# Kernel optimization log

Hardware: AMD Instinct MI355X
Metric: run time of the kernel (lower is better)

## Reference

```python
import jax, jax.numpy as jnp
import numpy as np
import math

D = 1024      # size_kernel
H = 16        # num_heads
HD = D // H   # head_dim
PAD = 1       # pad_index
B, S = 8, 1024


def setup_inputs() -> dict:
    key = jax.random.key(0)
    ks = jax.random.split(key, 10)
    scale = 1.0 / math.sqrt(D)
    x = jax.random.normal(ks[0], (B, S, D), dtype=jnp.float32)
    input_ids = jax.random.randint(ks[1], (B, S), 0, 10000, dtype=jnp.int64)
    Wq = jax.random.uniform(ks[2], (D, D), jnp.float32, -scale, scale)
    bq = jax.random.uniform(ks[3], (D,), jnp.float32, -scale, scale)
    Wk = jax.random.uniform(ks[4], (D, D), jnp.float32, -scale, scale)
    bk = jax.random.uniform(ks[5], (D,), jnp.float32, -scale, scale)
    Wv = jax.random.uniform(ks[6], (D, D), jnp.float32, -scale, scale)
    bv = jax.random.uniform(ks[7], (D,), jnp.float32, -scale, scale)
    Wo = jax.random.uniform(ks[8], (D, D), jnp.float32, -scale, scale)
    bo = jax.random.uniform(ks[9], (D,), jnp.float32, -scale, scale)
    return {"x": x, "input_ids": input_ids, "Wq": Wq, "bq": bq,
            "Wk": Wk, "bk": bk, "Wv": Wv, "bv": bv, "Wo": Wo, "bo": bo}


def reference(x, input_ids, Wq, bq, Wk, bk, Wv, bv, Wo, bo):
    b, s, _ = x.shape
    # QKV projections -> [b, h, s, hd]
    def split_heads(t):
        return t.reshape(b, s, H, HD).transpose(0, 2, 1, 3)
    q = split_heads(x @ Wq.T + bq)
    k = split_heads(x @ Wk.T + bk)
    v = split_heads(x @ Wv.T + bv)
    # scores [b, h, s, s]
    scores = jnp.einsum('bhqd,bhkd->bhqk', q, k) / math.sqrt(HD)
    pad_mask = (input_ids != PAD)[:, None, None, :]          # [b,1,1,s] keys
    causal = jnp.tril(jnp.ones((s, s), dtype=bool))[None, None]  # [1,1,s,s]
    mask = pad_mask & causal
    min_val = jnp.finfo(scores.dtype).min
    scores = jnp.where(mask, scores, min_val)
    attn = jax.nn.softmax(scores, axis=-1)
    out = jnp.einsum('bhqk,bhkd->bhqd', attn, v)             # [b,h,s,hd]
    out = out.transpose(0, 2, 1, 3).reshape(b, s, D)
    return out @ Wo.T + bo
```

## Files before the change

kernel.cpp:

```cpp
#include <hip/hip_runtime.h>

typedef __attribute__((ext_vector_type(8))) short bf16x8;
typedef __attribute__((ext_vector_type(8))) unsigned short u16x8;
typedef __attribute__((ext_vector_type(4))) unsigned short u16x4;
typedef __attribute__((ext_vector_type(4))) float f32x4;
typedef unsigned short u16t;

#define MFMA16(a, b, c) __builtin_amdgcn_mfma_f32_16x16x32_bf16((a), (b), (c), 0, 0, 0)
#define GLDS16(gp, lp)                                                        \
  __builtin_amdgcn_global_load_lds(                                           \
      (__attribute__((address_space(1))) void*)(gp),                          \
      (__attribute__((address_space(3))) void*)(lp), 16, 0, 0)

static constexpr float L2E = 1.44269504f;
static constexpr float MASKV = -1.0e30f;

__device__ __forceinline__ u16t f2b(float f) {
  unsigned u = __builtin_bit_cast(unsigned, f);
  u = u + 0x7fffu + ((u >> 16) & 1u);
  return (u16t)(u >> 16);
}

__global__ void cvt5(const float* __restrict__ x, const float* __restrict__ wq,
                     const float* __restrict__ wk, const float* __restrict__ wv,
                     const float* __restrict__ wo, u16t* __restrict__ xb,
                     u16t* __restrict__ wqb, u16t* __restrict__ wkb,
                     u16t* __restrict__ wvb, u16t* __restrict__ wob) {
  const int bid = blockIdx.x;
  const float* src; u16t* dst; int gb;
  if (bid < 4096)      { src = x;  dst = xb;  gb = bid; }
  else if (bid < 4608) { src = wq; dst = wqb; gb = bid - 4096; }
  else if (bid < 5120) { src = wk; dst = wkb; gb = bid - 4608; }
  else if (bid < 5632) { src = wv; dst = wvb; gb = bid - 5120; }
  else                 { src = wo; dst = wob; gb = bid - 5632; }
  const size_t i = (size_t)gb * 256 + threadIdx.x;
  const float4 a = ((const float4*)src)[2 * i];
  const float4 b = ((const float4*)src)[2 * i + 1];
  u16x8 r;
  r[0] = f2b(a.x); r[1] = f2b(a.y); r[2] = f2b(a.z); r[3] = f2b(a.w);
  r[4] = f2b(b.x); r[5] = f2b(b.y); r[6] = f2b(b.z); r[7] = f2b(b.w);
  *(u16x8*)&dst[8 * i] = r;
}

__global__ void gemm_qkv(const u16t* __restrict__ X,
                         const u16t* __restrict__ Wq, const u16t* __restrict__ Wk,
                         const u16t* __restrict__ Wv,
                         const float* __restrict__ bq, const float* __restrict__ bk,
                         const float* __restrict__ bv,
                         u16t* __restrict__ Qo, u16t* __restrict__ Ko,
                         u16t* __restrict__ Vo) {
  __shared__ __align__(16) u16t As[128 * 32];
  __shared__ __align__(16) u16t Bs[128 * 32];
  const int t = threadIdx.x, lane = t & 63, w = t >> 6;
  const int wr = w >> 1, wc = w & 1, m = lane & 15, quad = lane >> 4;
  const int rowBase = blockIdx.y * 128, colBase = blockIdx.x * 128;
  const int z = blockIdx.z;
  const u16t* W = (z == 0) ? Wq : ((z == 1) ? Wk : Wv);
  const float* bias = (z == 0) ? bq : ((z == 1) ? bk : bv);
  u16t* Out = (z == 0) ? Qo : ((z == 1) ? Ko : Vo);

  f32x4 acc[4][4];
#pragma unroll
  for (int i = 0; i < 4; i++)
#pragma unroll
    for (int j = 0; j < 4; j++) acc[i][j] = (f32x4){0.f, 0.f, 0.f, 0.f};

  const int lr = lane >> 2, lc = (lane & 3) * 8;
  for (int kt = 0; kt < 32; ++kt) {
#pragma unroll
    for (int i = 0; i < 2; ++i) {
      const int r0 = i * 64 + w * 16;
      GLDS16(&X[(size_t)(rowBase + r0 + lr) * 1024 + kt * 32 + lc], &As[r0 * 32]);
      GLDS16(&W[(size_t)(colBase + r0 + lr) * 1024 + kt * 32 + lc], &Bs[r0 * 32]);
    }
    __syncthreads();
    bf16x8 af[4], bfr[4];
#pragma unroll
    for (int i = 0; i < 4; i++)
      af[i] = *(const bf16x8*)&As[(wr * 64 + i * 16 + m) * 32 + quad * 8];
#pragma unroll
    for (int j = 0; j < 4; j++)
      bfr[j] = *(const bf16x8*)&Bs[(wc * 64 + j * 16 + m) * 32 + quad * 8];
#pragma unroll
    for (int i = 0; i < 4; i++)
#pragma unroll
      for (int j = 0; j < 4; j++) acc[i][j] = MFMA16(af[i], bfr[j], acc[i][j]);
    __syncthreads();
  }

  const int b_ = rowBase >> 10;
  const int sBase = (rowBase & 1023) + wr * 64;
#pragma unroll
  for (int j = 0; j < 4; j++) {
    const int col = colBase + wc * 64 + j * 16 + m;
    const float bv_ = bias[col];
    const int h = col >> 6, hd = col & 63;
    if (z == 2) {
#pragma unroll
      for (int i = 0; i < 4; i++) {
        const int s0 = sBase + i * 16 + quad * 4;
        u16x4 pk;
#pragma unroll
        for (int r = 0; r < 4; r++) pk[r] = f2b(acc[i][j][r] + bv_);
        *(u16x4*)&Out[(((size_t)b_ * 16 + h) * 64 + hd) * 1024 + s0] = pk;
      }
    } else {
#pragma unroll
      for (int i = 0; i < 4; i++) {
#pragma unroll
        for (int r = 0; r < 4; r++) {
          const int s_ = sBase + i * 16 + quad * 4 + r;
          const size_t oi = (((size_t)b_ * 16 + h) * 1024 + s_) * 64 + hd;
          Out[oi] = f2b(acc[i][j][r] + bv_);
        }
      }
    }
  }
}

__global__ void gemm_o(const u16t* __restrict__ A, const u16t* __restrict__ W,
                       const float* __restrict__ bias, float* __restrict__ Out) {
  __shared__ __align__(16) u16t As[128 * 32];
  __shared__ __align__(16) u16t Bs[128 * 32];
  const int t = threadIdx.x, lane = t & 63, w = t >> 6;
  const int wr = w >> 1, wc = w & 1, m = lane & 15, quad = lane >> 4;
  const int rowBase = blockIdx.y * 128, colBase = blockIdx.x * 128;

  f32x4 acc[4][4];
#pragma unroll
  for (int i = 0; i < 4; i++)
#pragma unroll
    for (int j = 0; j < 4; j++) acc[i][j] = (f32x4){0.f, 0.f, 0.f, 0.f};

  const int lr = lane >> 2, lc = (lane & 3) * 8;
  for (int kt = 0; kt < 32; ++kt) {
#pragma unroll
    for (int i = 0; i < 2; ++i) {
      const int r0 = i * 64 + w * 16;
      GLDS16(&A[(size_t)(rowBase + r0 + lr) * 1024 + kt * 32 + lc], &As[r0 * 32]);
      GLDS16(&W[(size_t)(colBase + r0 + lr) * 1024 + kt * 32 + lc], &Bs[r0 * 32]);
    }
    __syncthreads();
    bf16x8 af[4], bfr[4];
#pragma unroll
    for (int i = 0; i < 4; i++)
      af[i] = *(const bf16x8*)&As[(wr * 64 + i * 16 + m) * 32 + quad * 8];
#pragma unroll
    for (int j = 0; j < 4; j++)
      bfr[j] = *(const bf16x8*)&Bs[(wc * 64 + j * 16 + m) * 32 + quad * 8];
#pragma unroll
    for (int i = 0; i < 4; i++)
#pragma unroll
      for (int j = 0; j < 4; j++) acc[i][j] = MFMA16(af[i], bfr[j], acc[i][j]);
    __syncthreads();
  }

#pragma unroll
  for (int j = 0; j < 4; j++) {
    const int col = colBase + wc * 64 + j * 16 + m;
    const float bv_ = bias[col];
#pragma unroll
    for (int i = 0; i < 4; i++) {
#pragma unroll
      for (int r = 0; r < 4; r++) {
        const int row = rowBase + wr * 64 + i * 16 + quad * 4 + r;
        Out[(size_t)row * 1024 + col] = acc[i][j][r] + bv_;
      }
    }
  }
}

__global__ __launch_bounds__(512) void attn(
    const u16t* __restrict__ Q, const u16t* __restrict__ K,
    const u16t* __restrict__ VT, const int* __restrict__ ids,
    u16t* __restrict__ Oo) {
  constexpr int PSTR = 72;
  __shared__ __align__(16) u16t Kb[2][64 * 64];
  __shared__ __align__(16) u16t Vb[2][64 * 64];
  __shared__ __align__(16) u16t Ps[8][16 * PSTR];
  __shared__ unsigned long long maskL[16];

  const int t = threadIdx.x, lane = t & 63, wl = t >> 6;
  const int m = lane & 15, quad = lane >> 4;
  const int id = blockIdx.x;
  const int g = id & 7, k_ = id >> 3;
  const int bh = g + 8 * (k_ & 15);
  const int p4 = k_ >> 4;
  const int b = bh >> 4, h = bh & 15;
  const size_t hoff = (size_t)bh * 65536;

  const int srow = lane >> 3;
  const int sg = (lane & 7) ^ (srow & 7);

#pragma unroll
  for (int c = 0; c < 2; ++c) {
    const int chunk = wl * 2 + c;
    const int idv = ids[b * 1024 + chunk * 64 + lane];
    const unsigned long long mk = __ballot(idv != 1);
    if (lane == 0) maskL[chunk] = mk;
  }
  __syncthreads();

  u16t* const Pw = &Ps[wl][0];

  for (int pass = 0; pass < 2; ++pass) {
    const int qt8 = pass ? (7 - p4) : p4;
    const int qbase = qt8 * 128 + wl * 16;
    const int qrow = qbase + m;
    const int ktmax = 2 * qt8 + 1;

    GLDS16(&K[hoff + (size_t)(wl * 8 + srow) * 64 + sg * 8], &Kb[0][wl * 512]);
    GLDS16(&VT[hoff + (size_t)(wl * 8 + srow) * 1024 + sg * 8], &Vb[0][wl * 512]);

    const bf16x8 qf0 =
        *(const bf16x8*)&Q[hoff + (size_t)(qbase + m) * 64 + quad * 8];
    const bf16x8 qf1 =
        *(const bf16x8*)&Q[hoff + (size_t)(qbase + m) * 64 + 32 + quad * 8];

    float mi = MASKV, li = 0.f;
    f32x4 o[4];
#pragma unroll
    for (int ot = 0; ot < 4; ot++) o[ot] = (f32x4){0.f, 0.f, 0.f, 0.f};

    __syncthreads();

    for (int kt = 0; kt <= ktmax; ++kt) {
      if (kt < ktmax) {
        u16t* const kb = &Kb[(kt + 1) & 1][wl * 512];
        u16t* const vb = &Vb[(kt + 1) & 1][wl * 512];
        GLDS16(&K[hoff + (size_t)((kt + 1) * 64 + wl * 8 + srow) * 64 + sg * 8], kb);
        GLDS16(&VT[hoff + (size_t)(wl * 8 + srow) * 1024 + (kt + 1) * 64 + sg * 8], vb);
      }

      if (kt * 64 <= qbase + 15) {
        const u16t* const Kc = Kb[kt & 1];
        const u16t* const Vc = Vb[kt & 1];

        const int dq0 = qrow - kt * 64;
        const int dqc = dq0 > 63 ? 63 : dq0;
        const unsigned long long causal =
            (dqc == 63) ? ~0ull : ((1ull << (dqc + 1)) - 1ull);
        const unsigned long long km2 = maskL[kt] & causal;
        const unsigned kqlo = (unsigned)(km2 >> (quad * 4));
        const unsigned kqhi = (unsigned)(km2 >> (quad * 4 + 32));

        f32x4 sc[4];
        float pm = MASKV;
#pragma unroll
        for (int nt = 0; nt < 4; nt++) {
          if ((kt * 64 + nt * 16) <= (qbase + 15)) {
            const int krow = (nt * 16 + m) * 64;
            const bf16x8 k0 =
                *(const bf16x8*)&Kc[krow + ((quad ^ (m & 7)) & 7) * 8];
            const bf16x8 k1 =
                *(const bf16x8*)&Kc[krow + (((quad + 4) ^ (m & 7)) & 7) * 8];
            f32x4 c = (f32x4){0.f, 0.f, 0.f, 0.f};
            c = MFMA16(k0, qf0, c);
            c = MFMA16(k1, qf1, c);
            const unsigned w32 = (nt < 2) ? kqlo : kqhi;
#pragma unroll
            for (int r = 0; r < 4; r++) {
              const int sh = (nt & 1) * 16 + r;
              const float s = ((w32 >> sh) & 1u) ? c[r] * 0.125f : MASKV;
              sc[nt][r] = s;
              pm = fmaxf(pm, s);
            }
          } else {
#pragma unroll
            for (int r = 0; r < 4; r++) sc[nt][r] = MASKV;
          }
        }
        pm = fmaxf(pm, __shfl_xor(pm, 16));
        pm = fmaxf(pm, __shfl_xor(pm, 32));

        if (__any(pm > mi + 8.0f)) {
          const float mn = (pm > mi + 8.0f) ? pm : mi;
          const float alpha = exp2f((mi - mn) * L2E);
          mi = mn;
          li *= alpha;
#pragma unroll
          for (int r = 0; r < 4; r++) {
            const float ar = __shfl(alpha, quad * 4 + r);
#pragma unroll
            for (int ot = 0; ot < 4; ot++) o[ot][r] *= ar;
          }
        }

        float rsum = 0.f;
#pragma unroll
        for (int nt = 0; nt < 4; nt++) {
          float pf[4];
#pragma unroll
          for (int r = 0; r < 4; r++) {
            pf[r] = exp2f((sc[nt][r] - mi) * L2E);
            rsum += pf[r];
          }
          unsigned w0, w1;
          asm("v_cvt_pk_bf16_f32 %0, %1, %2" : "=v"(w0) : "v"(pf[0]), "v"(pf[1]));
          asm("v_cvt_pk_bf16_f32 %0, %1, %2" : "=v"(w1) : "v"(pf[2]), "v"(pf[3]));
          uint2 wv; wv.x = w0; wv.y = w1;
          *(uint2*)&Pw[m * PSTR + nt * 16 + quad * 4] = wv;
        }
        rsum += __shfl_xor(rsum, 16);
        rsum += __shfl_xor(rsum, 32);
        li += rsum;

        const bf16x8 p0 = *(const bf16x8*)&Pw[m * PSTR + quad * 8];
        const bf16x8 p1 = *(const bf16x8*)&Pw[m * PSTR + 32 + quad * 8];
#pragma unroll
        for (int ot = 0; ot < 4; ot++) {
          const int vrow = (ot * 16 + m) * 64;
          const bf16x8 v0 =
              *(const bf16x8*)&Vc[vrow + ((quad ^ (m & 7)) & 7) * 8];
          const bf16x8 v1 =
              *(const bf16x8*)&Vc[vrow + (((quad + 4) ^ (m & 7)) & 7) * 8];
          o[ot] = MFMA16(p0, v0, o[ot]);
          o[ot] = MFMA16(p1, v1, o[ot]);
        }
      }

      __syncthreads();
    }

    const float linv = (li > 1e-30f) ? 1.f / li : 0.f;
#pragma unroll
    for (int r = 0; r < 4; r++) {
      const float inv = __shfl(linv, quad * 4 + r);
      const int qo = qbase + quad * 4 + r;
#pragma unroll
      for (int ot = 0; ot < 4; ot++) {
        const int col = h * 64 + ot * 16 + m;
        Oo[((size_t)(b * 1024 + qo)) * 1024 + col] = f2b(o[ot][r] * inv);
      }
    }
  }
}

extern "C" void kernel_launch(void* const* d_in, const int* in_sizes, int n_in,
                              void* d_out, int out_size, void* d_ws, size_t ws_size,
                              hipStream_t stream) {
  const float* x  = (const float*)d_in[0];
  const int*   ids = (const int*)d_in[1];
  const float* Wq = (const float*)d_in[2];
  const float* bq = (const float*)d_in[3];
  const float* Wk = (const float*)d_in[4];
  const float* bk = (const float*)d_in[5];
  const float* Wv = (const float*)d_in[6];
  const float* bv = (const float*)d_in[7];
  const float* Wo = (const float*)d_in[8];
  const float* bo = (const float*)d_in[9];
  float* out = (float*)d_out;

  u16t* XB  = (u16t*)d_ws;
  u16t* WqB = XB  + 8388608;
  u16t* WkB = WqB + 1048576;
  u16t* WvB = WkB + 1048576;
  u16t* WoB = WvB + 1048576;
  u16t* Qw  = WoB + 1048576;
  u16t* Kw  = Qw  + 8388608;
  u16t* Vw  = Kw  + 8388608;
  u16t* AO  = XB;

  cvt5<<<6144, 256, 0, stream>>>(x, Wq, Wk, Wv, Wo, XB, WqB, WkB, WvB, WoB);
  gemm_qkv<<<dim3(8, 64, 3), 256, 0, stream>>>(XB, WqB, WkB, WvB, bq, bk, bv,
                                               Qw, Kw, Vw);
  attn<<<512, 512, 0, stream>>>(Qw, Kw, Vw, ids, AO);
  gemm_o<<<dim3(8, 64, 1), 256, 0, stream>>>(AO, WoB, bo, out);
}
```

Before: 265.3 us.

## Double-buffer GEMM LDS tiles and remap blocks for XCD-local L2 reuse

Both the QKV and output-projection GEMMs now keep two LDS buffers, issuing the global-to-LDS loads for the next K tile before computing on the current one. This drops one barrier per iteration and overlaps load latency with MFMA work. The grids are flattened to 1D and remapped so that blocks landing on the same XCD share row tiles, aiming to improve L2 reuse of the A operand. The cost is double the LDS per block, which could lower occupancy.

```diff
diff --git a/kernel.cpp b/kernel.cpp
--- a/kernel.cpp
+++ b/kernel.cpp
@@ -49,12 +49,16 @@
                          const float* __restrict__ bv,
                          u16t* __restrict__ Qo, u16t* __restrict__ Ko,
                          u16t* __restrict__ Vo) {
-  __shared__ __align__(16) u16t As[128 * 32];
-  __shared__ __align__(16) u16t Bs[128 * 32];
+  __shared__ __align__(16) u16t As[2][128 * 32];
+  __shared__ __align__(16) u16t Bs[2][128 * 32];
   const int t = threadIdx.x, lane = t & 63, w = t >> 6;
   const int wr = w >> 1, wc = w & 1, m = lane & 15, quad = lane >> 4;
-  const int rowBase = blockIdx.y * 128, colBase = blockIdx.x * 128;
-  const int z = blockIdx.z;
+  const int id = blockIdx.x;
+  const int xcd = id & 7, j = id >> 3;
+  const int by = xcd * 8 + (j & 7);
+  const int rem = j >> 3;
+  const int bx = rem & 7, z = rem >> 3;
+  const int rowBase = by * 128, colBase = bx * 128;
   const u16t* W = (z == 0) ? Wq : ((z == 1) ? Wk : Wv);
   const float* bias = (z == 0) ? bq : ((z == 1) ? bk : bv);
   u16t* Out = (z == 0) ? Qo : ((z == 1) ? Ko : Vo);
@@ -63,36 +67,48 @@
 #pragma unroll
   for (int i = 0; i < 4; i++)
 #pragma unroll
-    for (int j = 0; j < 4; j++) acc[i][j] = (f32x4){0.f, 0.f, 0.f, 0.f};
+    for (int j2 = 0; j2 < 4; j2++) acc[i][j2] = (f32x4){0.f, 0.f, 0.f, 0.f};
 
   const int lr = lane >> 2, lc = (lane & 3) * 8;
+#pragma unroll
+  for (int i = 0; i < 2; ++i) {
+    const int r0 = i * 64 + w * 16;
+    GLDS16(&X[(size_t)(rowBase + r0 + lr) * 1024 + lc], &As[0][r0 * 32]);
+    GLDS16(&W[(size_t)(colBase + r0 + lr) * 1024 + lc], &Bs[0][r0 * 32]);
+  }
+  __syncthreads();
+
   for (int kt = 0; kt < 32; ++kt) {
-#pragma unroll
-    for (int i = 0; i < 2; ++i) {
-      const int r0 = i * 64 + w * 16;
-      GLDS16(&X[(size_t)(rowBase + r0 + lr) * 1024 + kt * 32 + lc], &As[r0 * 32]);
-      GLDS16(&W[(size_t)(colBase + r0 + lr) * 1024 + kt * 32 + lc], &Bs[r0 * 32]);
-    }
-    __syncthreads();
+    const int cur = kt & 1;
+    if (kt < 31) {
+#pragma unroll
+      for (int i = 0; i < 2; ++i) {
+        const int r0 = i * 64 + w * 16;
+        GLDS16(&X[(size_t)(rowBase + r0 + lr) * 1024 + (kt + 1) * 32 + lc],
+               &As[cur ^ 1][r0 * 32]);
+        GLDS16(&W[(size_t)(colBase + r0 + lr) * 1024 + (kt + 1) * 32 + lc],
+               &Bs[cur ^ 1][r0 * 32]);
+      }
+    }
     bf16x8 af[4], bfr[4];
 #pragma unroll
     for (int i = 0; i < 4; i++)
-      af[i] = *(const bf16x8*)&As[(wr * 64 + i * 16 + m) * 32 + quad * 8];
-#pragma unroll
-    for (int j = 0; j < 4; j++)
-      bfr[j] = *(const bf16x8*)&Bs[(wc * 64 + j * 16 + m) * 32 + quad * 8];
+      af[i] = *(const bf16x8*)&As[cur][(wr * 64 + i * 16 + m) * 32 + quad * 8];
+#pragma unroll
+    for (int j2 = 0; j2 < 4; j2++)
+      bfr[j2] = *(const bf16x8*)&Bs[cur][(wc * 64 + j2 * 16 + m) * 32 + quad * 8];
 #pragma unroll
     for (int i = 0; i < 4; i++)
 #pragma unroll
-      for (int j = 0; j < 4; j++) acc[i][j] = MFMA16(af[i], bfr[j], acc[i][j]);
+      for (int j2 = 0; j2 < 4; j2++) acc[i][j2] = MFMA16(af[i], bfr[j2], acc[i][j2]);
     __syncthreads();
   }
 
   const int b_ = rowBase >> 10;
   const int sBase = (rowBase & 1023) + wr * 64;
 #pragma unroll
-  for (int j = 0; j < 4; j++) {
-    const int col = colBase + wc * 64 + j * 16 + m;
+  for (int j2 = 0; j2 < 4; j2++) {
+    const int col = colBase + wc * 64 + j2 * 16 + m;
     const float bv_ = bias[col];
     const int h = col >> 6, hd = col & 63;
     if (z == 2) {
@@ -101,7 +117,7 @@
         const int s0 = sBase + i * 16 + quad * 4;
         u16x4 pk;
 #pragma unroll
-        for (int r = 0; r < 4; r++) pk[r] = f2b(acc[i][j][r] + bv_);
+        for (int r = 0; r < 4; r++) pk[r] = f2b(acc[i][j2][r] + bv_);
         *(u16x4*)&Out[(((size_t)b_ * 16 + h) * 64 + hd) * 1024 + s0] = pk;
       }
     } else {
@@ -111,7 +127,7 @@
         for (int r = 0; r < 4; r++) {
           const int s_ = sBase + i * 16 + quad * 4 + r;
           const size_t oi = (((size_t)b_ * 16 + h) * 1024 + s_) * 64 + hd;
-          Out[oi] = f2b(acc[i][j][r] + bv_);
+          Out[oi] = f2b(acc[i][j2][r] + bv_);
         }
       }
     }
@@ -120,51 +136,67 @@
 
 __global__ void gemm_o(const u16t* __restrict__ A, const u16t* __restrict__ W,
                        const float* __restrict__ bias, float* __restrict__ Out) {
-  __shared__ __align__(16) u16t As[128 * 32];
-  __shared__ __align__(16) u16t Bs[128 * 32];
+  __shared__ __align__(16) u16t As[2][128 * 32];
+  __shared__ __align__(16) u16t Bs[2][128 * 32];
   const int t = threadIdx.x, lane = t & 63, w = t >> 6;
   const int wr = w >> 1, wc = w & 1, m = lane & 15, quad = lane >> 4;
-  const int rowBase = blockIdx.y * 128, colBase = blockIdx.x * 128;
+  const int id = blockIdx.x;
+  const int xcd = id & 7, j = id >> 3;
+  const int by = xcd * 8 + (j & 7);
+  const int bx = j >> 3;
+  const int rowBase = by * 128, colBase = bx * 128;
 
   f32x4 acc[4][4];
 #pragma unroll
   for (int i = 0; i < 4; i++)
 #pragma unroll
-    for (int j = 0; j < 4; j++) acc[i][j] = (f32x4){0.f, 0.f, 0.f, 0.f};
+    for (int j2 = 0; j2 < 4; j2++) acc[i][j2] = (f32x4){0.f, 0.f, 0.f, 0.f};
 
   const int lr = lane >> 2, lc = (lane & 3) * 8;
+#pragma unroll
+  for (int i = 0; i < 2; ++i) {
+    const int r0 = i * 64 + w * 16;
+    GLDS16(&A[(size_t)(rowBase + r0 + lr) * 1024 + lc], &As[0][r0 * 32]);
+    GLDS16(&W[(size_t)(colBase + r0 + lr) * 1024 + lc], &Bs[0][r0 * 32]);
+  }
+  __syncthreads();
+
   for (int kt = 0; kt < 32; ++kt) {
-#pragma unroll
-    for (int i = 0; i < 2; ++i) {
-      const int r0 = i * 64 + w * 16;
-      GLDS16(&A[(size_t)(rowBase + r0 + lr) * 1024 + kt * 32 + lc], &As[r0 * 32]);
-      GLDS16(&W[(size_t)(colBase + r0 + lr) * 1024 + kt * 32 + lc], &Bs[r0 * 32]);
-    }
+    const int cur = kt & 1;
+    if (kt < 31) {
+#pragma unroll
+      for (int i = 0; i < 2; ++i) {
+        const int r0 = i * 64 + w * 16;
+        GLDS16(&A[(size_t)(rowBase + r0 + lr) * 1024 + (kt + 1) * 32 + lc],
+               &As[cur ^ 1][r0 * 32]);
+        GLDS16(&W[(size_t)(colBase + r0 + lr) * 1024 + (kt + 1) * 32 + lc],
+               &Bs[cur ^ 1][r0 * 32]);
+      }
+    }
+    bf16x8 af[4], bfr[4];
+#pragma unroll
+    for (int i = 0; i < 4; i++)
+      af[i] = *(const bf16x8*)&As[cur][(wr * 64 + i * 16 + m) * 32 + quad * 8];
+#pragma unroll
+    for (int j2 = 0; j2 < 4; j2++)
+      bfr[j2] = *(const bf16x8*)&Bs[cur][(wc * 64 + j2 * 16 + m) * 32 + quad * 8];
+#pragma unroll
+    for (int i = 0; i < 4; i++)
+#pragma unroll
+      for (int j2 = 0; j2 < 4; j2++) acc[i][j2] = MFMA16(af[i], bfr[j2], acc[i][j2]);
     __syncthreads();
-    bf16x8 af[4], bfr[4];
-#pragma unroll
-    for (int i = 0; i < 4; i++)
-      af[i] = *(const bf16x8*)&As[(wr * 64 + i * 16 + m) * 32 + quad * 8];
-#pragma unroll
-    for (int j = 0; j < 4; j++)
-      bfr[j] = *(const bf16x8*)&Bs[(wc * 64 + j * 16 + m) * 32 + quad * 8];
-#pragma unroll
-    for (int i = 0; i < 4; i++)
-#pragma unroll
-      for (int j = 0; j < 4; j++) acc[i][j] = MFMA16(af[i], bfr[j], acc[i][j]);
-    __syncthreads();
-  }
-
-#pragma unroll
-  for (int j = 0; j < 4; j++) {
-    const int col = colBase + wc * 64 + j * 16 + m;
+  }
+
+#pragma unroll
+  for (int j2 = 0; j2 < 4; j2++) {
+    const int col = colBase + wc * 64 + j2 * 16 + m;
     const float bv_ = bias[col];
 #pragma unroll
     for (int i = 0; i < 4; i++) {
 #pragma unroll
       for (int r = 0; r < 4; r++) {
         const int row = rowBase + wr * 64 + i * 16 + quad * 4 + r;
-        Out[(size_t)row * 1024 + col] = acc[i][j][r] + bv_;
+        Out[(size_t)row * 1024 + col] = acc[i][j2][r] + bv_;
       }
     }
   }
@@ -362,8 +394,7 @@
   u16t* AO  = XB;
 
   cvt5<<<6144, 256, 0, stream>>>(x, Wq, Wk, Wv, Wo, XB, WqB, WkB, WvB, WoB);
-  gemm_qkv<<<dim3(8, 64, 3), 256, 0, stream>>>(XB, WqB, WkB, WvB, bq, bk, bv,
-                                               Qw, Kw, Vw);
+  gemm_qkv<<<1536, 256, 0, stream>>>(XB, WqB, WkB, WvB, bq, bk, bv, Qw, Kw, Vw);
   attn<<<512, 512, 0, stream>>>(Qw, Kw, Vw, ids, AO);
-  gemm_o<<<dim3(8, 64, 1), 256, 0, stream>>>(AO, WoB, bo, out);
-}
+  gemm_o<<<512, 256, 0, stream>>>(AO, WoB, bo, out);
+}
```

Result: faster. 254.3 us (-4.1%).
